# Performance work log

Measured on AMD Instinct MI355X. Metric: run time of the kernel, lower is better.

Reference implementation:

```python
import jax, jax.numpy as jnp
import numpy as np

B, S, D = 4, 2048, 2048
D_INNER = max(128, D // 2)  # 1024, torch default d_inner
FO = 2                      # filter_order
K = 3                       # kernel_size
KS = 3                      # short_kernel_size


def setup_inputs() -> dict:
    key = jax.random.key(0)
    ks = jax.random.split(key, 6)
    return {
        "x": jax.random.normal(ks[0], (B, S, D), jnp.float32),
        # depthwise short conv: weight (D, KS), bias (D,)
        "short_w": jax.random.normal(ks[1], (D, KS), jnp.float32) / np.float32(np.sqrt(KS)),
        "short_b": jnp.zeros((D,), jnp.float32),
        # filter MLP proj: Linear(D -> FO*D_INNER)
        "proj_w": jax.random.normal(ks[2], (D, FO * D_INNER), jnp.float32) / np.float32(np.sqrt(D)),
        "proj_b": jnp.zeros((FO * D_INNER,), jnp.float32),
        # filter MLP output: Linear(D_INNER -> K), SHARED across filter orders
        "filt_w": jax.random.normal(ks[3], (D_INNER, K), jnp.float32) / np.float32(np.sqrt(D_INNER)),
        "filt_b": jnp.zeros((K,), jnp.float32),
        # output projection Linear(D -> D)
        "out_w": jax.random.normal(ks[4], (D, D), jnp.float32) / np.float32(np.sqrt(D)),
        "out_b": jnp.zeros((D,), jnp.float32),
    }


def reference(x, short_w, short_b, proj_w, proj_b, filt_w, filt_b, out_w, out_b):
    b, s, d = x.shape
    v = x  # v captured BEFORE short-conv residual, as in the torch code

    # --- causal depthwise short conv (pad k-1 on left, truncate to s) ---
    xp = jnp.pad(x, ((0, 0), (KS - 1, 0), (0, 0)))
    x_short = short_b
    for j in range(KS):  # tiny fixed kernel loop
        x_short = x_short + xp[:, j:j + s, :] * short_w[:, j]
    x = x + x_short

    # --- filter function: Linear -> GELU -> (shared) Linear -> tanh ---
    h = jax.nn.gelu(x @ proj_w + proj_b, approximate=False)         # (b, s, FO*D_INNER)
    h = h.reshape(b, s, FO, D_INNER)
    filt = jnp.tanh(jnp.einsum('bsfi,ik->bsfk', h, filt_w) + filt_b)  # (b, s, FO, K)

    # --- gated depthwise conv: kernel = mean over seq, shared across channels;
    # sum over filter orders commutes with the (linear) conv, so fold it in ---
    w = filt.mean(axis=1).sum(axis=1)                                # (b, K)
    xp2 = jnp.pad(x, ((0, 0), (K - 1, 0), (0, 0)))
    conv = jnp.zeros_like(x)
    for j in range(K):
        conv = conv + xp2[:, j:j + s, :] * w[:, j][:, None, None]

    # --- gate with v, GELU, output projection ---
    y = jax.nn.gelu(conv * v, approximate=False)
    return y @ out_w + out_b
```

## Files before the change

kernel.cpp:

```cpp
#include <hip/hip_runtime.h>
#include <hip/hip_bf16.h>
#include <math.h>

typedef unsigned short u16;
typedef __attribute__((ext_vector_type(4))) unsigned short u16x4;
typedef __attribute__((ext_vector_type(8))) unsigned short u16x8;
typedef __attribute__((ext_vector_type(8))) short s16x8;
typedef __attribute__((ext_vector_type(4))) float f32x4;

#define B_  4
#define S_  2048
#define D_  2048
#define DI_ 1024
#define MROWS (B_ * S_)
#define KDIM  D_
#define NDIM  D_
#define STRIP 16

__device__ __forceinline__ float b2f(u16 u) {
    union { unsigned i; float f; } v; v.i = ((unsigned)u) << 16; return v.f;
}
__device__ __forceinline__ u16 f2b(float f) {
    unsigned u = __float_as_uint(f);
    unsigned r = (u + 0x7FFFu + ((u >> 16) & 1u)) >> 16;
    return (u16)r;
}
__device__ __forceinline__ float gelu_exact(float x) {
    return 0.5f * x * (1.0f + erff(x * 0.70710678118654752f));
}

#define GLOAD_LDS16(gp, lp)                                                    \
    __builtin_amdgcn_global_load_lds(                                          \
        (const __attribute__((address_space(1))) void*)(gp),                   \
        (__attribute__((address_space(3))) void*)(lp), 16, 0, 0)

__global__ void transpose_k(const float* __restrict__ in0, u16* __restrict__ out0,
                            const float* __restrict__ in1, u16* __restrict__ out1,
                            int n) {
    __shared__ float tile[32][33];
    const float* in = (blockIdx.z == 0) ? in0 : in1;
    u16* out = (blockIdx.z == 0) ? out0 : out1;
    int bx = blockIdx.x * 32, by = blockIdx.y * 32;
    int tx = threadIdx.x, ty = threadIdx.y;
    for (int i = 0; i < 32; i += 8)
        tile[ty + i][tx] = in[(size_t)(by + ty + i) * n + bx + tx];
    __syncthreads();
    for (int i = 0; i < 32; i += 8)
        out[(size_t)(bx + ty + i) * n + by + tx] = f2b(tile[tx][ty + i]);
}

__global__ void shortconv_k(const float* __restrict__ x, const float* __restrict__ sw,
                            const float* __restrict__ sb, u16* __restrict__ xs,
                            float* __restrict__ wacc, float* __restrict__ t_g) {
    const int bid = blockIdx.y * 2 + blockIdx.x;
    {
        int z = bid * 256 + threadIdx.x;
        if (z < 12) wacc[z] = 0.0f;
        if (z < MROWS * 6) t_g[z] = 0.0f;
    }
    const int c = blockIdx.x * 1024 + threadIdx.x * 4;
    const int r0 = blockIdx.y * STRIP;
    const int t0 = r0 & (S_ - 1);

    float tap[12];
    #pragma unroll
    for (int q = 0; q < 3; ++q)
        ((f32x4*)tap)[q] = *(const f32x4*)(sw + (size_t)c * 3 + q * 4);
    f32x4 sbv = *(const f32x4*)(sb + c);

    const float* base = x + (size_t)r0 * D_ + c;
    f32x4 m2, m1;
    if (t0 == 0) { m2 = (f32x4)(0.0f); m1 = (f32x4)(0.0f); }
    else { m2 = *(const f32x4*)(base - 2 * D_); m1 = *(const f32x4*)(base - D_); }

    u16* op = xs + (size_t)r0 * D_ + c;
    #pragma unroll
    for (int rr = 0; rr < STRIP; ++rr) {
        f32x4 cur = *(const f32x4*)(base + (size_t)rr * D_);
        u16x4 outv;
        #pragma unroll
        for (int e = 0; e < 4; ++e) {
            float v = cur[e] + sbv[e]
                    + tap[e * 3 + 0] * m2[e]
                    + tap[e * 3 + 1] * m1[e]
                    + tap[e * 3 + 2] * cur[e];
            outv[e] = f2b(v);
        }
        *(u16x4*)(op + (size_t)rr * D_) = outv;
        m2 = m1; m1 = cur;
    }
}

#define STG_A(REG, KOFF) do { const u16* _g = gA + (KOFF);                     \
    GLOAD_LDS16(_g, &As[REG][ldsW0]);                                          \
    GLOAD_LDS16(_g + (size_t)128 * KDIM, &As[REG][ldsW1]); } while (0)
#define STG_B(REG, KOFF) do { const u16* _g = gB + (KOFF);                     \
    GLOAD_LDS16(_g, &Bs[REG][ldsW0]);                                          \
    GLOAD_LDS16(_g + (size_t)128 * KDIM, &Bs[REG][ldsW1]); } while (0)
#define LD_B4(REG) do {                                                        \
    bf[0] = *(const s16x8*)&Bs[REG][boffR[0]];                                 \
    bf[1] = *(const s16x8*)&Bs[REG][boffR[1]];                                 \
    bf[2] = *(const s16x8*)&Bs[REG][boffR[2]];                                 \
    bf[3] = *(const s16x8*)&Bs[REG][boffR[3]]; } while (0)
#define LD_A4(REG, I0) do {                                                    \
    af[0] = *(const s16x8*)&As[REG][aoffR[(I0) + 0]];                          \
    af[1] = *(const s16x8*)&As[REG][aoffR[(I0) + 1]];                          \
    af[2] = *(const s16x8*)&As[REG][aoffR[(I0) + 2]];                          \
    af[3] = *(const s16x8*)&As[REG][aoffR[(I0) + 3]]; } while (0)
#define SYNC_IN() do { __builtin_amdgcn_s_barrier();                           \
    asm volatile("s_waitcnt lgkmcnt(0)" ::: "memory");                         \
    __builtin_amdgcn_sched_barrier(0); } while (0)
#define MFMA16(I0) do { __builtin_amdgcn_s_setprio(1);                         \
    _Pragma("unroll")                                                          \
    for (int i_ = 0; i_ < 4; ++i_) {                                           \
        _Pragma("unroll")                                                      \
        for (int j_ = 0; j_ < 4; ++j_)                                         \
            acc[(I0) + i_][j_] = __builtin_amdgcn_mfma_f32_16x16x32_bf16(      \
                af[i_], bf[j_], acc[(I0) + i_][j_], 0, 0, 0);                  \
    }                                                                          \
    __builtin_amdgcn_s_setprio(0); } while (0)
#define BARR() __builtin_amdgcn_s_barrier()
#define VM8() asm volatile("s_waitcnt vmcnt(8)" ::: "memory")
#define VM4() asm volatile("s_waitcnt vmcnt(4)" ::: "memory")
#define VM0() asm volatile("s_waitcnt vmcnt(0)" ::: "memory")

#define GEMM_CORE(APTR, BPTR)                                                  \
    __shared__ u16 As[4][8192];                                                \
    __shared__ u16 Bs[4][8192];                                                \
    const int tid  = threadIdx.x;                                              \
    const int wid  = tid >> 6;                                                 \
    const int lane = tid & 63;                                                 \
    const int wr   = wid >> 2;                                                 \
    const int wc   = wid & 3;                                                  \
    const int row0 = blockIdx.y << 8;                                          \
    const int col0 = blockIdx.x << 8;                                          \
    const int rowS    = tid >> 2;                                              \
    const int colOffS = (((tid & 3) ^ ((rowS >> 1) & 3)) << 3);                \
    const u16* gA = (APTR) + (size_t)(row0 + rowS) * KDIM + colOffS;           \
    const u16* gB = (BPTR) + (size_t)(col0 + rowS) * KDIM + colOffS;           \
    const int ldsW0 = wid * 512;                                               \
    const int ldsW1 = 4096 + wid * 512;                                        \
    int aoffR[8], boffR[4];                                                    \
    _Pragma("unroll")                                                          \
    for (int i = 0; i < 8; ++i) {                                              \
        int row  = (wr << 7) + (i << 4) + (lane & 15);                         \
        int slot = (lane >> 4) ^ ((row >> 1) & 3);                             \
        aoffR[i] = row * 32 + slot * 8;                                        \
    }                                                                          \
    _Pragma("unroll")                                                          \
    for (int j = 0; j < 4; ++j) {                                              \
        int row  = (wc << 6) + (j << 4) + (lane & 15);                         \
        int slot = (lane >> 4) ^ ((row >> 1) & 3);                             \
        boffR[j] = row * 32 + slot * 8;                                        \
    }                                                                          \
    f32x4 acc[8][4];                                                           \
    _Pragma("unroll")                                                          \
    for (int i = 0; i < 8; ++i)                                                \
        _Pragma("unroll")                                                      \
        for (int j = 0; j < 4; ++j) acc[i][j] = (f32x4)(0.0f);                 \
    s16x8 af[4], bf[4];                                                        \
    STG_A(0, 0);  STG_B(0, 0);                                                 \
    STG_A(1, 32); STG_B(1, 32);                                                \
    STG_A(2, 64); STG_B(2, 64);                                                \
    VM8();                                                                     \
    BARR();                                                                    \
    _Pragma("unroll 1")                                                        \
    for (int t = 0; t < 15; ++t) {                                             \
        const int kb = t * 128;                                                \
        LD_B4(0); LD_A4(0,0); STG_A(3, kb + 96);  SYNC_IN(); MFMA16(0); BARR();        \
        LD_A4(0,4);           STG_B(3, kb + 96);  SYNC_IN(); MFMA16(4); VM8(); BARR(); \
        LD_B4(1); LD_A4(1,0); STG_A(0, kb + 128); SYNC_IN(); MFMA16(0); BARR();        \
        LD_A4(1,4);           STG_B(0, kb + 128); SYNC_IN(); MFMA16(4); VM8(); BARR(); \
        LD_B4(2); LD_A4(2,0); STG_A(1, kb + 160); SYNC_IN(); MFMA16(0); BARR();        \
        LD_A4(2,4);           STG_B(1, kb + 160); SYNC_IN(); MFMA16(4); VM8(); BARR(); \
        LD_B4(3); LD_A4(3,0); STG_A(2, kb + 192); SYNC_IN(); MFMA16(0); BARR();        \
        LD_A4(3,4);           STG_B(2, kb + 192); SYNC_IN(); MFMA16(4); VM8(); BARR(); \
    }                                                                          \
    {                                                                          \
        const int kb = 15 * 128;                                               \
        LD_B4(0); LD_A4(0,0); STG_A(3, kb + 96);  SYNC_IN(); MFMA16(0); BARR();        \
        LD_A4(0,4);           STG_B(3, kb + 96);  SYNC_IN(); MFMA16(4); VM8(); BARR(); \
        LD_B4(1); LD_A4(1,0);                     SYNC_IN(); MFMA16(0); BARR();        \
        LD_A4(1,4);                               SYNC_IN(); MFMA16(4); VM4(); BARR(); \
        LD_B4(2); LD_A4(2,0);                     SYNC_IN(); MFMA16(0); BARR();        \
        LD_A4(2,4);                               SYNC_IN(); MFMA16(4); VM0(); BARR(); \
        LD_B4(3); LD_A4(3,0);                     SYNC_IN(); MFMA16(0); BARR();        \
        LD_A4(3,4);                               SYNC_IN(); MFMA16(4); BARR();        \
    }

__global__ __launch_bounds__(512, 2)
void gemm_f8(const u16* __restrict__ A, const u16* __restrict__ BT,
             const float* __restrict__ bias,
             const float* __restrict__ fw, float* __restrict__ t_g) {
    GEMM_CORE(A, BT)

    __shared__ float t_lds[768];
    __syncthreads();
    for (int z = tid; z < 768; z += 512) t_lds[z] = 0.0f;
    __syncthreads();

    const int colt0 = (wc << 6) + (lane & 15);
    float fwv[4][3], bsv[4];
    const int ibase = (col0 & (DI_ - 1)) + colt0;
    #pragma unroll
    for (int j = 0; j < 4; ++j) {
        int ifilt = ibase + j * 16;
        fwv[j][0] = fw[ifilt * 3 + 0];
        fwv[j][1] = fw[ifilt * 3 + 1];
        fwv[j][2] = fw[ifilt * 3 + 2];
        bsv[j] = bias[col0 + colt0 + j * 16];
    }
    #pragma unroll
    for (int i = 0; i < 8; ++i) {
        #pragma unroll
        for (int r = 0; r < 4; ++r) {
            float s0 = 0.f, s1 = 0.f, s2 = 0.f;
            #pragma unroll
            for (int j = 0; j < 4; ++j) {
                float hv = gelu_exact(acc[i][j][r] + bsv[j]);
                s0 += hv * fwv[j][0];
                s1 += hv * fwv[j][1];
                s2 += hv * fwv[j][2];
            }
            #pragma unroll
            for (int m = 1; m < 16; m <<= 1) {
                s0 += __shfl_xor(s0, m, 16);
                s1 += __shfl_xor(s1, m, 16);
                s2 += __shfl_xor(s2, m, 16);
            }
            if ((lane & 15) == 0) {
                int trow = (wr << 7) + ((lane >> 4) << 2) + (i << 4) + r;
                atomicAdd(&t_lds[trow * 3 + 0], s0);
                atomicAdd(&t_lds[trow * 3 + 1], s1);
                atomicAdd(&t_lds[trow * 3 + 2], s2);
            }
        }
    }
    __syncthreads();
    const int f3 = (col0 >= DI_) ? 3 : 0;
    for (int z = tid; z < 768; z += 512) {
        int rr = z / 3, k = z - rr * 3;
        atomicAdd(&t_g[(size_t)(row0 + rr) * 6 + f3 + k], t_lds[z]);
    }
}

__global__ __launch_bounds__(512, 2)
void gemm8_k(const u16* __restrict__ A, const u16* __restrict__ BT,
             const float* __restrict__ bias, float* __restrict__ C) {
    GEMM_CORE(A, BT)

    const int colt0 = (wc << 6) + (lane & 15);
    const int crow0 = row0 + (wr << 7) + ((lane >> 4) << 2);
    #pragma unroll
    for (int j = 0; j < 4; ++j) {
        int col = col0 + colt0 + j * 16;
        float bs = bias[col];
        #pragma unroll
        for (int i = 0; i < 8; ++i) {
            int rbase = crow0 + i * 16;
            #pragma unroll
            for (int r = 0; r < 4; ++r)
                C[(size_t)(rbase + r) * NDIM + col] = acc[i][j][r] + bs;
        }
    }
}

__global__ void filt_finish_k(const float* __restrict__ t_g, const float* __restrict__ fb,
                              float* __restrict__ wacc) {
    __shared__ float part[3];
    const int tid = threadIdx.x;
    if (tid < 3) part[tid] = 0.0f;
    __syncthreads();
    int p = blockIdx.x * 256 + tid;
    int row = p >> 1, f = p & 1;
    const float* tp = t_g + (size_t)row * 6 + f * 3;
    atomicAdd(&part[0], tanhf(tp[0] + fb[0]));
    atomicAdd(&part[1], tanhf(tp[1] + fb[1]));
    atomicAdd(&part[2], tanhf(tp[2] + fb[2]));
    __syncthreads();
    if (tid < 3) {
        int b = blockIdx.x >> 4;
        atomicAdd(&wacc[b * 3 + tid], part[tid]);
    }
}

__global__ void gate_k(const u16* __restrict__ xs, const float* __restrict__ v,
                       const float* __restrict__ wacc, u16* __restrict__ g) {
    const int c = blockIdx.x * 1024 + threadIdx.x * 4;
    const int r0 = blockIdx.y * STRIP;
    const int t0 = r0 & (S_ - 1);
    const int b = r0 >> 11;
    const float w0 = wacc[b * 3 + 0] * (1.0f / (float)S_);
    const float w1 = wacc[b * 3 + 1] * (1.0f / (float)S_);
    const float w2 = wacc[b * 3 + 2] * (1.0f / (float)S_);

    const u16* base = xs + (size_t)r0 * D_ + c;
    f32x4 m2, m1;
    if (t0 == 0) {
        m2 = (f32x4)(0.0f); m1 = (f32x4)(0.0f);
    } else {
        u16x4 a2 = *(const u16x4*)(base - 2 * D_);
        u16x4 a1 = *(const u16x4*)(base - D_);
        #pragma unroll
        for (int e = 0; e < 4; ++e) { m2[e] = b2f(a2[e]); m1[e] = b2f(a1[e]); }
    }

    const float* vp = v + (size_t)r0 * D_ + c;
    u16* op = g + (size_t)r0 * D_ + c;
    #pragma unroll
    for (int rr = 0; rr < STRIP; ++rr) {
        u16x4 cb = *(const u16x4*)(base + (size_t)rr * D_);
        f32x4 vv = *(const f32x4*)(vp + (size_t)rr * D_);
        f32x4 cur;
        #pragma unroll
        for (int e = 0; e < 4; ++e) cur[e] = b2f(cb[e]);
        u16x4 outv;
        #pragma unroll
        for (int e = 0; e < 4; ++e) {
            float conv = w0 * m2[e] + w1 * m1[e] + w2 * cur[e];
            outv[e] = f2b(gelu_exact(conv * vv[e]));
        }
        *(u16x4*)(op + (size_t)rr * D_) = outv;
        m2 = m1; m1 = cur;
    }
}

extern "C" void kernel_launch(void* const* d_in, const int* in_sizes, int n_in,
                              void* d_out, int out_size, void* d_ws, size_t ws_size,
                              hipStream_t stream) {
    const float* x       = (const float*)d_in[0];
    const float* short_w = (const float*)d_in[1];
    const float* short_b = (const float*)d_in[2];
    const float* proj_w  = (const float*)d_in[3];
    const float* proj_b  = (const float*)d_in[4];
    const float* filt_w  = (const float*)d_in[5];
    const float* filt_b  = (const float*)d_in[6];
    const float* out_w   = (const float*)d_in[7];
    const float* out_b   = (const float*)d_in[8];
    float* out = (float*)d_out;

    char* ws = (char*)d_ws;
    const size_t xs_bytes = (size_t)MROWS * D_ * 2;
    const size_t wt_bytes = (size_t)KDIM * NDIM * 2;
    float* wacc = (float*)(ws);
    float* t_g  = (float*)(ws + 1024);
    u16*   xs   = (u16*)(ws + 262144);
    u16*   g    = (u16*)(ws + 262144 + xs_bytes);
    u16*   wT1  = (u16*)(ws + 262144 + 2 * xs_bytes);
    const size_t need_dual = 262144 + 2 * xs_bytes + 2 * wt_bytes;
    const bool dual = (ws_size >= need_dual);
    u16* wT2 = dual ? (u16*)(ws + 262144 + 2 * xs_bytes + wt_bytes) : wT1;

    dim3 tb(32, 8, 1);

    if (dual) {
        dim3 tg(D_ / 32, D_ / 32, 2);
        transpose_k<<<tg, tb, 0, stream>>>(proj_w, wT1, out_w, wT2, D_);
    } else {
        dim3 tg(D_ / 32, D_ / 32, 1);
        transpose_k<<<tg, tb, 0, stream>>>(proj_w, wT1, proj_w, wT1, D_);
    }

    dim3 cg(2, MROWS / STRIP, 1);
    shortconv_k<<<cg, 256, 0, stream>>>(x, short_w, short_b, xs, wacc, t_g);

    dim3 gg(NDIM / 256, MROWS / 256, 1);
    gemm_f8<<<gg, 512, 0, stream>>>(xs, wT1, proj_b, filt_w, t_g);

    filt_finish_k<<<64, 256, 0, stream>>>(t_g, filt_b, wacc);

    if (!dual) {
        dim3 tg(D_ / 32, D_ / 32, 1);
        transpose_k<<<tg, tb, 0, stream>>>(out_w, wT2, out_w, wT2, D_);
    }

    gate_k<<<cg, 256, 0, stream>>>(xs, x, wacc, g);

    gemm8_k<<<gg, 512, 0, stream>>>(g, wT2, out_b, out);
}
```

Measured before the change: 362.0 us.

## Software-pipeline LDS fragment loads with MFMA in GEMM main loop

Restructures the GEMM core so LDS fragment loads for the next k-slice (A low half and B) are double-buffered in registers and issued while the current MFMAs run. The A high half is loaded during the low-half MFMAs. This drops the explicit lgkmcnt(0) wait before each MFMA batch and halves barriers per sub-tile. The aim is to hide LDS latency behind matrix math. It costs extra VGPRs for the double buffers, which may pressure occupancy at 512 threads x 2 blocks. It also relies on compiler-inserted waits being correct.

```diff
diff --git a/kernel.cpp b/kernel.cpp
--- a/kernel.cpp
+++ b/kernel.cpp
@@ -97,34 +97,57 @@
 #define STG_B(REG, KOFF) do { const u16* _g = gB + (KOFF);                     \
     GLOAD_LDS16(_g, &Bs[REG][ldsW0]);                                          \
     GLOAD_LDS16(_g + (size_t)128 * KDIM, &Bs[REG][ldsW1]); } while (0)
-#define LD_B4(REG) do {                                                        \
-    bf[0] = *(const s16x8*)&Bs[REG][boffR[0]];                                 \
-    bf[1] = *(const s16x8*)&Bs[REG][boffR[1]];                                 \
-    bf[2] = *(const s16x8*)&Bs[REG][boffR[2]];                                 \
-    bf[3] = *(const s16x8*)&Bs[REG][boffR[3]]; } while (0)
-#define LD_A4(REG, I0) do {                                                    \
-    af[0] = *(const s16x8*)&As[REG][aoffR[(I0) + 0]];                          \
-    af[1] = *(const s16x8*)&As[REG][aoffR[(I0) + 1]];                          \
-    af[2] = *(const s16x8*)&As[REG][aoffR[(I0) + 2]];                          \
-    af[3] = *(const s16x8*)&As[REG][aoffR[(I0) + 3]]; } while (0)
-#define SYNC_IN() do { __builtin_amdgcn_s_barrier();                           \
-    asm volatile("s_waitcnt lgkmcnt(0)" ::: "memory");                         \
-    __builtin_amdgcn_sched_barrier(0); } while (0)
-#define MFMA16(I0) do { __builtin_amdgcn_s_setprio(1);                         \
+#define LD_AH(R_) do {                                                         \
+    aH[0] = *(const s16x8*)&As[R_][aoffR[4]];                                  \
+    aH[1] = *(const s16x8*)&As[R_][aoffR[5]];                                  \
+    aH[2] = *(const s16x8*)&As[R_][aoffR[6]];                                  \
+    aH[3] = *(const s16x8*)&As[R_][aoffR[7]]; } while (0)
+#define LD_ALBC(S_, R_) do {                                                   \
+    aL[S_][0] = *(const s16x8*)&As[R_][aoffR[0]];                              \
+    aL[S_][1] = *(const s16x8*)&As[R_][aoffR[1]];                              \
+    aL[S_][2] = *(const s16x8*)&As[R_][aoffR[2]];                              \
+    aL[S_][3] = *(const s16x8*)&As[R_][aoffR[3]];                              \
+    bC[S_][0] = *(const s16x8*)&Bs[R_][boffR[0]];                              \
+    bC[S_][1] = *(const s16x8*)&Bs[R_][boffR[1]];                              \
+    bC[S_][2] = *(const s16x8*)&Bs[R_][boffR[2]];                              \
+    bC[S_][3] = *(const s16x8*)&Bs[R_][boffR[3]]; } while (0)
+#define MFMA_LO(S_) do { __builtin_amdgcn_s_setprio(1);                        \
     _Pragma("unroll")                                                          \
     for (int i_ = 0; i_ < 4; ++i_) {                                           \
         _Pragma("unroll")                                                      \
         for (int j_ = 0; j_ < 4; ++j_)                                         \
-            acc[(I0) + i_][j_] = __builtin_amdgcn_mfma_f32_16x16x32_bf16(      \
-                af[i_], bf[j_], acc[(I0) + i_][j_], 0, 0, 0);                  \
+            acc[i_][j_] = __builtin_amdgcn_mfma_f32_16x16x32_bf16(             \
+                aL[S_][i_], bC[S_][j_], acc[i_][j_], 0, 0, 0);                 \
+    }                                                                          \
+    __builtin_amdgcn_s_setprio(0); } while (0)
+#define MFMA_HI(S_) do { __builtin_amdgcn_s_setprio(1);                        \
+    _Pragma("unroll")                                                          \
+    for (int i_ = 0; i_ < 4; ++i_) {                                           \
+        _Pragma("unroll")                                                      \
+        for (int j_ = 0; j_ < 4; ++j_)                                         \
+            acc[4 + i_][j_] = __builtin_amdgcn_mfma_f32_16x16x32_bf16(         \
+                aH[i_], bC[S_][j_], acc[4 + i_][j_], 0, 0, 0);                 \
     }                                                                          \
     __builtin_amdgcn_s_setprio(0); } while (0)
 #define BARR() __builtin_amdgcn_s_barrier()
 #define VM8() asm volatile("s_waitcnt vmcnt(8)" ::: "memory")
 #define VM4() asm volatile("s_waitcnt vmcnt(4)" ::: "memory")
 #define VM0() asm volatile("s_waitcnt vmcnt(0)" ::: "memory")
-
-#define GEMM_CORE(APTR, BPTR)                                                  \
+#define VMNOP()
+
+#define TILE(T_, R_, RN_, CS_, NS_, DOSTG_, GATE_, DOPF_) do {                 \
+    BARR();                                                                    \
+    if (DOSTG_) { STG_A((((R_) + 3) & 3), ((T_) + 3) * 32);                    \
+                  STG_B((((R_) + 3) & 3), ((T_) + 3) * 32); }                  \
+    LD_AH(R_);                                                                 \
+    MFMA_LO(CS_);                                                              \
+    GATE_;                                                                     \
+    BARR();                                                                    \
+    if (DOPF_) { LD_ALBC(NS_, RN_); }                                          \
+    MFMA_HI(CS_);                                                              \
+} while (0)
+
+#define GEMM_CORE_OL(APTR, BPTR)                                               \
     __shared__ u16 As[4][8192];                                                \
     __shared__ u16 Bs[4][8192];                                                \
     const int tid  = threadIdx.x;                                              \
@@ -158,41 +181,31 @@
     for (int i = 0; i < 8; ++i)                                                \
         _Pragma("unroll")                                                      \
         for (int j = 0; j < 4; ++j) acc[i][j] = (f32x4)(0.0f);                 \
-    s16x8 af[4], bf[4];                                                        \
+    s16x8 aL[2][4], bC[2][4], aH[4];                                           \
     STG_A(0, 0);  STG_B(0, 0);                                                 \
     STG_A(1, 32); STG_B(1, 32);                                                \
     STG_A(2, 64); STG_B(2, 64);                                                \
-    VM8();                                                                     \
+    VM8();                          \
     BARR();                                                                    \
+    LD_ALBC(0, 0);                                       \
     _Pragma("unroll 1")                                                        \
     for (int t = 0; t < 15; ++t) {                                             \
-        const int kb = t * 128;                                                \
-        LD_B4(0); LD_A4(0,0); STG_A(3, kb + 96);  SYNC_IN(); MFMA16(0); BARR();        \
-        LD_A4(0,4);           STG_B(3, kb + 96);  SYNC_IN(); MFMA16(4); VM8(); BARR(); \
-        LD_B4(1); LD_A4(1,0); STG_A(0, kb + 128); SYNC_IN(); MFMA16(0); BARR();        \
-        LD_A4(1,4);           STG_B(0, kb + 128); SYNC_IN(); MFMA16(4); VM8(); BARR(); \
-        LD_B4(2); LD_A4(2,0); STG_A(1, kb + 160); SYNC_IN(); MFMA16(0); BARR();        \
-        LD_A4(2,4);           STG_B(1, kb + 160); SYNC_IN(); MFMA16(4); VM8(); BARR(); \
-        LD_B4(3); LD_A4(3,0); STG_A(2, kb + 192); SYNC_IN(); MFMA16(0); BARR();        \
-        LD_A4(3,4);           STG_B(2, kb + 192); SYNC_IN(); MFMA16(4); VM8(); BARR(); \
-    }                                                                          \
-    {                                                                          \
-        const int kb = 15 * 128;                                               \
-        LD_B4(0); LD_A4(0,0); STG_A(3, kb + 96);  SYNC_IN(); MFMA16(0); BARR();        \
-        LD_A4(0,4);           STG_B(3, kb + 96);  SYNC_IN(); MFMA16(4); VM8(); BARR(); \
-        LD_B4(1); LD_A4(1,0);                     SYNC_IN(); MFMA16(0); BARR();        \
-        LD_A4(1,4);                               SYNC_IN(); MFMA16(4); VM4(); BARR(); \
-        LD_B4(2); LD_A4(2,0);                     SYNC_IN(); MFMA16(0); BARR();        \
-        LD_A4(2,4);                               SYNC_IN(); MFMA16(4); VM0(); BARR(); \
-        LD_B4(3); LD_A4(3,0);                     SYNC_IN(); MFMA16(0); BARR();        \
-        LD_A4(3,4);                               SYNC_IN(); MFMA16(4); BARR();        \
-    }
+        const int T4 = t * 4;                                                  \
+        TILE(T4 + 0, 0, 1, 0, 1, 1, VM8(), 1);                                 \
+        TILE(T4 + 1, 1, 2, 1, 0, 1, VM8(), 1);                                 \
+        TILE(T4 + 2, 2, 3, 0, 1, 1, VM8(), 1);                                 \
+        TILE(T4 + 3, 3, 0, 1, 0, 1, VM8(), 1);                                 \
+    }                                                                          \
+    TILE(60, 0, 1, 0, 1, 1, VM8(), 1);                                         \
+    TILE(61, 1, 2, 1, 0, 0, VM4(), 1);                                         \
+    TILE(62, 2, 3, 0, 1, 0, VM0(), 1);                                         \
+    TILE(63, 3, 0, 1, 0, 0, VMNOP(), 0);
 
 __global__ __launch_bounds__(512, 2)
 void gemm_f8(const u16* __restrict__ A, const u16* __restrict__ BT,
              const float* __restrict__ bias,
              const float* __restrict__ fw, float* __restrict__ t_g) {
-    GEMM_CORE(A, BT)
+    GEMM_CORE_OL(A, BT)
 
     __shared__ float t_lds[768];
     __syncthreads();
@@ -247,7 +260,7 @@
 __global__ __launch_bounds__(512, 2)
 void gemm8_k(const u16* __restrict__ A, const u16* __restrict__ BT,
              const float* __restrict__ bias, float* __restrict__ C) {
-    GEMM_CORE(A, BT)
+    GEMM_CORE_OL(A, BT)
 
     const int colt0 = (wc << 6) + (lane & 15);
     const int crow0 = row0 + (wr << 7) + ((lane >> 4) << 2);
```

After: 360.2 us. About the same (-0.5%).
